# Kernel tuning notes

Hardware: AMD Instinct MI355X
Metric: run time of the kernel (lower is better)

Reference implementation:

```python
import jax, jax.numpy as jnp
import numpy as np

# Config derived from init_kwargs
DIM = 256
DSTATE = 64
DCONV = 3
HEADDIM = 64
CHUNK = 256
NGROUPS = 1
DINNER = int(2.0 * DIM)                 # 512
NHEADS = DINNER // HEADDIM              # 8
CONVDIM = DINNER + 2 * NGROUPS * DSTATE  # 640 (x, B, C share the depthwise conv)
DPROJ = 2 * DINNER + 2 * NGROUPS * DSTATE + NHEADS  # z + xBC + dt


def setup_inputs() -> dict:
    key = jax.random.key(0)
    ks = jax.random.split(key, 8)
    B, H, W = 8, 64, 64
    return dict(
        x=jax.random.normal(ks[0], (B, DIM, H, W), jnp.float32),
        ln_w=jnp.ones((DIM,), jnp.float32),
        ln_b=jnp.zeros((DIM,), jnp.float32),
        in_proj_w=jax.random.normal(ks[1], (DPROJ, DIM), jnp.float32) * 0.02,
        conv_w=jax.random.normal(ks[2], (CONVDIM, 1, DCONV, DCONV), jnp.float32) * 0.1,
        conv_b=jnp.zeros((CONVDIM,), jnp.float32),
        A_log=jnp.log(jax.random.uniform(ks[3], (NHEADS,), jnp.float32, 1.0, 16.0)),
        D=jnp.ones((NHEADS,), jnp.float32),
        dt_bias=jax.random.uniform(ks[4], (NHEADS,), jnp.float32, -2.0, 0.0),
        rms_w=jnp.ones((DINNER,), jnp.float32),
        out_proj_w=jax.random.normal(ks[5], (DIM, DINNER), jnp.float32) * 0.02,
    )


def _ssd(X, dA, Bm, Cm, chunk):
    """Mamba2 SSD chunked parallel scan.
    X:  (b, l, h, p)  inputs already multiplied by dt
    dA: (b, l, h)     dt * A (negative)
    Bm, Cm: (b, l, h, n)
    """
    b, l, h, p = X.shape
    n = Bm.shape[-1]
    c = l // chunk
    q = chunk
    Xc = X.reshape(b, c, q, h, p)
    Bc = Bm.reshape(b, c, q, h, n)
    Cc = Cm.reshape(b, c, q, h, n)
    Ac = dA.reshape(b, c, q, h).transpose(0, 3, 1, 2)            # (b,h,c,q)
    Acs = jnp.cumsum(Ac, axis=-1)                                # (b,h,c,q)
    # intra-chunk (diagonal blocks): causal decay matrix L
    tri = jnp.tril(jnp.ones((q, q), bool))
    Ldec = jnp.where(tri, jnp.exp(Acs[..., :, None] - Acs[..., None, :]), 0.0)
    Y_diag = jnp.einsum('bcqhn,bcshn,bhcqs,bcshp->bcqhp', Cc, Bc, Ldec, Xc)
    # per-chunk final states
    decay_states = jnp.exp(Acs[..., -1:] - Acs)                  # (b,h,c,q)
    states = jnp.einsum('bcqhn,bhcq,bcqhp->bchpn', Bc, decay_states, Xc)
    # inter-chunk recurrence (segment-sum over chunk totals)
    A_last = jnp.pad(Acs[..., -1], ((0, 0), (0, 0), (1, 0)))     # (b,h,c+1)
    ccs = jnp.cumsum(A_last, axis=-1)
    tric = jnp.tril(jnp.ones((c + 1, c + 1), bool))
    decay_chunk = jnp.where(tric, jnp.exp(ccs[..., :, None] - ccs[..., None, :]), 0.0)
    states0 = jnp.concatenate([jnp.zeros_like(states[:, :1]), states], axis=1)
    prev = jnp.einsum('bhzc,bchpn->bzhpn', decay_chunk, states0)[:, :-1]
    # contribution of carried-in state (off-diagonal blocks)
    Y_off = jnp.einsum('bcqhn,bchpn,bhcq->bcqhp', Cc, prev, jnp.exp(Acs))
    return (Y_diag + Y_off).reshape(b, l, h, p)


def _forward(x, ln_w, ln_b, in_proj_w, conv_w, conv_b, A_log, D, dt_bias, rms_w, out_proj_w):
    Bn, Cd, Hh, Ww = x.shape
    L = Hh * Ww
    # LayerNorm over channel dim (channel-first LayerNorm2d)
    mu = jnp.mean(x, axis=1, keepdims=True)
    var = jnp.mean((x - mu) ** 2, axis=1, keepdims=True)
    xn = (x - mu) * jax.lax.rsqrt(var + 1e-5)
    xn = xn * ln_w[None, :, None, None] + ln_b[None, :, None, None]
    # input projection (1x1): -> z | xBC | dt
    zxbcdt = jnp.einsum('bchw,dc->bdhw', xn, in_proj_w)
    z = zxbcdt[:, :DINNER]
    xBC = zxbcdt[:, DINNER:DINNER + CONVDIM]
    dt = zxbcdt[:, DINNER + CONVDIM:]                            # (b, nheads, H, W)
    # depthwise 2D conv + SiLU on xBC
    xBC = jax.lax.conv_general_dilated(
        xBC, conv_w, (1, 1), 'SAME',
        dimension_numbers=('NCHW', 'OIHW', 'NCHW'), feature_group_count=CONVDIM)
    xBC = jax.nn.silu(xBC + conv_b[None, :, None, None])
    # flatten spatial -> sequence, channel-last
    def to_seq(t):
        return t.reshape(Bn, t.shape[1], L).transpose(0, 2, 1)
    xBC, dt, z = to_seq(xBC), to_seq(dt), to_seq(z)
    xs = xBC[..., :DINNER].reshape(Bn, L, NHEADS, HEADDIM)
    Bg = xBC[..., DINNER:DINNER + NGROUPS * DSTATE].reshape(Bn, L, NGROUPS, DSTATE)
    Cg = xBC[..., DINNER + NGROUPS * DSTATE:].reshape(Bn, L, NGROUPS, DSTATE)
    hpg = NHEADS // NGROUPS
    Bm = jnp.repeat(Bg, hpg, axis=2)
    Cm = jnp.repeat(Cg, hpg, axis=2)
    dt = jax.nn.softplus(dt + dt_bias[None, None, :])            # (b, L, nheads)
    A = -jnp.exp(A_log)
    y = _ssd(xs * dt[..., None], dt * A[None, None, :], Bm, Cm, CHUNK)
    y = y + D[None, None, :, None] * xs                          # skip connection
    y = y.reshape(Bn, L, DINNER)
    # gated RMSNorm: norm(y * silu(z)) * w
    y = y * jax.nn.silu(z)
    y = y * jax.lax.rsqrt(jnp.mean(y * y, axis=-1, keepdims=True) + 1e-5) * rms_w
    out = jnp.einsum('bld,cd->blc', y, out_proj_w)
    out = out.transpose(0, 2, 1).reshape(Bn, Cd, Hh, Ww)
    return x + out                                               # residual


def reference(x, ln_w, ln_b, in_proj_w, conv_w, conv_b, A_log, D, dt_bias, rms_w, out_proj_w):
    return _forward(x, ln_w, ln_b, in_proj_w, conv_w, conv_b, A_log, D, dt_bias, rms_w, out_proj_w)
```

## Files before the change

kernel.cpp:

```cpp
#include <hip/hip_runtime.h>
#include <hip/hip_bf16.h>
#include <math.h>

#define DIMC   256
#define LSP    4096
#define BATCH  8
#define DINNER 512
#define NHEADS 8
#define HEADDIM 64
#define DSTATE 64
#define CONVDIM 640
#define DPROJ  1160
#define MPAD   1280
#define CHUNK  256
#define NCHUNK 16

typedef unsigned short u16;
typedef __attribute__((ext_vector_type(8))) unsigned short u16x8;
typedef __attribute__((ext_vector_type(8))) short s16x8;
typedef __attribute__((ext_vector_type(4))) float f32x4;

#define MFMA16(a,b,c) __builtin_amdgcn_mfma_f32_16x16x32_bf16((s16x8)(a),(s16x8)(b),(c),0,0,0)

__device__ __forceinline__ float bf2f(u16 u){ return __uint_as_float(((unsigned int)u)<<16); }
__device__ __forceinline__ u16 f2bf(float f){
  unsigned int x = __float_as_uint(f);
  unsigned int r = (x + 0x7fffu + ((x>>16)&1u)) >> 16;
  return (u16)r;
}
__device__ __forceinline__ float softplusf(float x){ return (x > 20.f) ? x : log1pf(expf(x)); }
__device__ __forceinline__ float siluf(float x){ return x / (1.f + expf(-x)); }
__device__ __forceinline__ u16x8 fscale(u16x8 v, float s){
  u16x8 r;
  #pragma unroll
  for(int j=0;j<8;j++) r[j] = f2bf(bf2f(v[j])*s);
  return r;
}

__global__ void convert_w(const float* __restrict__ src, u16* __restrict__ dst,
                          int total, int valid){
  int i = blockIdx.x*256 + threadIdx.x;
  if (i >= total) return;
  dst[i] = (i < valid) ? f2bf(src[i]) : (u16)0;
}

__global__ void ln_kernel(const float* __restrict__ X, const float* __restrict__ lnw,
                          const float* __restrict__ lnb, u16* __restrict__ XNT) {
  int pos = blockIdx.x*256 + threadIdx.x;
  int b = pos >> 12, l = pos & (LSP-1);
  const float* xb = X + ((size_t)b*DIMC)*LSP + l;
  float sum=0.f, sq=0.f;
  for (int c=0;c<DIMC;c++){ float v=xb[(size_t)c*LSP]; sum+=v; sq+=v*v; }
  float mu = sum*(1.f/DIMC);
  float var = sq*(1.f/DIMC) - mu*mu;
  float rs = rsqrtf(var + 1e-5f);
  u16* ob = XNT + ((size_t)(b*LSP + l))*DIMC;
  for (int c0=0;c0<DIMC;c0+=8){
    u16x8 v8;
    #pragma unroll
    for(int j=0;j<8;j++){
      float v = xb[(size_t)(c0+j)*LSP];
      v8[j] = f2bf((v-mu)*rs*lnw[c0+j] + lnb[c0+j]);
    }
    *(u16x8*)&ob[c0] = v8;
  }
}

__global__ void gemm_zt_mfma(const u16* __restrict__ W, const u16* __restrict__ Bm,
                             u16* __restrict__ ZT){
  __shared__ u16 As[128][32];
  __shared__ u16 Bs[128][32];
  int tid=threadIdx.x, w=tid>>6, lane=tid&63, l15=lane&15, quad=lane>>4;
  int b=blockIdx.z, m0=blockIdx.y*128, n0=blockIdx.x*128;
  const u16* Ab = Bm + ((size_t)b*LSP + m0)*DIMC;
  f32x4 acc[4][4];
  #pragma unroll
  for(int i=0;i<4;i++)
    #pragma unroll
    for(int j=0;j<4;j++) acc[i][j] = (f32x4){0.f,0.f,0.f,0.f};
  for (int k0=0;k0<DIMC;k0+=32){
    __syncthreads();
    {
      int ch = tid*2;
      int r = ch>>2, o=(ch&3)*8;
      *(u16x8*)&As[r][o] = *(const u16x8*)&Ab[(size_t)r*DIMC + k0 + o];
      *(u16x8*)&Bs[r][o] = *(const u16x8*)&W[(size_t)(n0+r)*DIMC + k0 + o];
      ch++; r = ch>>2; o=(ch&3)*8;
      *(u16x8*)&As[r][o] = *(const u16x8*)&Ab[(size_t)r*DIMC + k0 + o];
      *(u16x8*)&Bs[r][o] = *(const u16x8*)&W[(size_t)(n0+r)*DIMC + k0 + o];
    }
    __syncthreads();
    int mrow = (w>>1)*64, ncol=(w&1)*64;
    u16x8 af[4], bfr[4];
    #pragma unroll
    for(int mt=0;mt<4;mt++) af[mt] = *(const u16x8*)&As[mrow+mt*16+l15][quad*8];
    #pragma unroll
    for(int nt=0;nt<4;nt++) bfr[nt] = *(const u16x8*)&Bs[ncol+nt*16+l15][quad*8];
    #pragma unroll
    for(int mt=0;mt<4;mt++)
      #pragma unroll
      for(int nt=0;nt<4;nt++)
        acc[mt][nt]=MFMA16(af[mt],bfr[nt],acc[mt][nt]);
  }
  #pragma unroll
  for(int mt=0;mt<4;mt++)
    #pragma unroll
    for(int nt=0;nt<4;nt++)
      #pragma unroll
      for(int r=0;r<4;r++){
        int l = m0 + (w>>1)*64 + mt*16 + quad*4 + r;
        int d = n0 + (w&1)*64 + nt*16 + l15;
        ZT[((size_t)b*LSP + l)*DINNER + d] = f2bf(acc[mt][nt][r]);
      }
}

__global__ void gemm_xbcdt_mfma(const u16* __restrict__ A, const u16* __restrict__ Bm,
                                u16* __restrict__ XBC, u16* __restrict__ DT){
  __shared__ u16 As[128][32];
  __shared__ u16 Bs[128][32];
  int tid=threadIdx.x, w=tid>>6, lane=tid&63, l15=lane&15, quad=lane>>4;
  int b=blockIdx.z, m0=DINNER + blockIdx.y*128, n0=blockIdx.x*128;
  const u16* Bb = Bm + ((size_t)b*LSP + n0)*DIMC;
  f32x4 acc[4][4];
  #pragma unroll
  for(int i=0;i<4;i++)
    #pragma unroll
    for(int j=0;j<4;j++) acc[i][j] = (f32x4){0.f,0.f,0.f,0.f};
  for (int k0=0;k0<DIMC;k0+=32){
    __syncthreads();
    {
      int ch = tid*2;
      int r = ch>>2, o=(ch&3)*8;
      *(u16x8*)&As[r][o] = *(const u16x8*)&A[(size_t)(m0+r)*DIMC + k0 + o];
      *(u16x8*)&Bs[r][o] = *(const u16x8*)&Bb[(size_t)r*DIMC + k0 + o];
      ch++; r = ch>>2; o=(ch&3)*8;
      *(u16x8*)&As[r][o] = *(const u16x8*)&A[(size_t)(m0+r)*DIMC + k0 + o];
      *(u16x8*)&Bs[r][o] = *(const u16x8*)&Bb[(size_t)r*DIMC + k0 + o];
    }
    __syncthreads();
    int mrow = (w>>1)*64, ncol=(w&1)*64;
    u16x8 af[4], bfr[4];
    #pragma unroll
    for(int mt=0;mt<4;mt++) af[mt] = *(const u16x8*)&As[mrow+mt*16+l15][quad*8];
    #pragma unroll
    for(int nt=0;nt<4;nt++) bfr[nt] = *(const u16x8*)&Bs[ncol+nt*16+l15][quad*8];
    #pragma unroll
    for(int mt=0;mt<4;mt++)
      #pragma unroll
      for(int nt=0;nt<4;nt++)
        acc[mt][nt]=MFMA16(af[mt],bfr[nt],acc[mt][nt]);
  }
  #pragma unroll
  for(int mt=0;mt<4;mt++)
    #pragma unroll
    for(int nt=0;nt<4;nt++)
      #pragma unroll
      for(int r=0;r<4;r++){
        int row = m0 + (w>>1)*64 + mt*16 + quad*4 + r;
        if (row>=DPROJ) continue;
        int col = n0 + (w&1)*64 + nt*16 + l15;
        u16 v = f2bf(acc[mt][nt][r]);
        if (row<DINNER+CONVDIM)   XBC[((size_t)b*CONVDIM+(row-DINNER))*LSP+col]=v;
        else                      DT[((size_t)b*NHEADS+(row-DINNER-CONVDIM))*LSP+col]=v;
      }
}

__global__ void gemm_out_mfma(const u16* __restrict__ A, const u16* __restrict__ Bm,
                              const float* __restrict__ Res, float* __restrict__ Out){
  __shared__ u16 As[128][32];
  __shared__ u16 Bs[128][32];
  int tid=threadIdx.x, w=tid>>6, lane=tid&63, l15=lane&15, quad=lane>>4;
  int b=blockIdx.z, m0=blockIdx.y*128, n0=blockIdx.x*128;
  const u16* Bb = Bm + ((size_t)b*LSP + n0)*DINNER;
  f32x4 acc[4][4];
  #pragma unroll
  for(int i=0;i<4;i++)
    #pragma unroll
    for(int j=0;j<4;j++) acc[i][j] = (f32x4){0.f,0.f,0.f,0.f};
  for (int k0=0;k0<DINNER;k0+=32){
    __syncthreads();
    {
      int ch = tid*2;
      int r = ch>>2, o=(ch&3)*8;
      *(u16x8*)&As[r][o] = *(const u16x8*)&A[(size_t)(m0+r)*DINNER + k0 + o];
      *(u16x8*)&Bs[r][o] = *(const u16x8*)&Bb[(size_t)r*DINNER + k0 + o];
      ch++; r = ch>>2; o=(ch&3)*8;
      *(u16x8*)&As[r][o] = *(const u16x8*)&A[(size_t)(m0+r)*DINNER + k0 + o];
      *(u16x8*)&Bs[r][o] = *(const u16x8*)&Bb[(size_t)r*DINNER + k0 + o];
    }
    __syncthreads();
    int mrow = (w>>1)*64, ncol=(w&1)*64;
    u16x8 af[4], bfr[4];
    #pragma unroll
    for(int mt=0;mt<4;mt++) af[mt] = *(const u16x8*)&As[mrow+mt*16+l15][quad*8];
    #pragma unroll
    for(int nt=0;nt<4;nt++) bfr[nt] = *(const u16x8*)&Bs[ncol+nt*16+l15][quad*8];
    #pragma unroll
    for(int mt=0;mt<4;mt++)
      #pragma unroll
      for(int nt=0;nt<4;nt++)
        acc[mt][nt]=MFMA16(af[mt],bfr[nt],acc[mt][nt]);
  }
  #pragma unroll
  for(int mt=0;mt<4;mt++)
    #pragma unroll
    for(int nt=0;nt<4;nt++)
      #pragma unroll
      for(int r=0;r<4;r++){
        int row = m0 + (w>>1)*64 + mt*16 + quad*4 + r;
        int col = n0 + (w&1)*64 + nt*16 + l15;
        size_t oi = ((size_t)b*DIMC+row)*LSP+col;
        Out[oi] = acc[mt][nt][r] + Res[oi];
      }
}

__global__ void conv_kernel(u16* __restrict__ XBC, const float* __restrict__ CW,
                            const float* __restrict__ CB){
  int ch = blockIdx.x, b = blockIdx.y, tid = threadIdx.x;
  __shared__ float plane[66*66];
  u16* base = XBC + ((size_t)b*CONVDIM + ch)*LSP;
  for (int idx=tid; idx<66*66; idx+=256){
    int yy = idx/66 - 1, xx = idx%66 - 1;
    float v = 0.f;
    if (yy>=0 && yy<64 && xx>=0 && xx<64) v = bf2f(base[yy*64+xx]);
    plane[idx] = v;
  }
  float wg[9];
  #pragma unroll
  for (int t=0;t<9;t++) wg[t] = CW[ch*9+t];
  float bias = CB[ch];
  __syncthreads();
  for (int r=0;r<16;r++){
    int pix = tid + r*256;
    int y = pix>>6, x = pix&63;
    float s=0.f;
    #pragma unroll
    for(int dy=0;dy<3;dy++)
      #pragma unroll
      for(int dx=0;dx<3;dx++) s += plane[(y+dy)*66 + x+dx]*wg[dy*3+dx];
    base[pix] = f2bf(siluf(s + bias));
  }
}

__global__ void ssd_pre_kernel(const u16* __restrict__ DT, const float* __restrict__ A_log,
                               const float* __restrict__ dt_bias, float* __restrict__ ACS,
                               float* __restrict__ DTV, float* __restrict__ DASUM){
  int c=blockIdx.x, h=blockIdx.y, b=blockIdx.z, tid=threadIdx.x;
  __shared__ float acs[CHUNK];
  size_t base = ((size_t)b*NHEADS+h)*LSP + c*CHUNK + tid;
  float raw = bf2f(DT[base]);
  float dtv = softplusf(raw + dt_bias[h]);
  float Ah = -expf(A_log[h]);
  acs[tid] = dtv*Ah;
  __syncthreads();
  for(int o=1;o<256;o<<=1){
    float add=(tid>=o)?acs[tid-o]:0.f;
    __syncthreads(); acs[tid]+=add; __syncthreads();
  }
  ACS[base] = acs[tid];
  DTV[base] = dtv;
  if (tid==CHUNK-1) DASUM[((size_t)b*NHEADS+h)*NCHUNK+c] = acs[tid];
}

__global__ __launch_bounds__(256,4) void ssd_states_mfma(
    const float* __restrict__ ACS, const float* __restrict__ DTV,
    const float* __restrict__ DASUM, const u16* __restrict__ XBC,
    float* __restrict__ STATES){
  int c=blockIdx.x, h=blockIdx.y, b=blockIdx.z;
  int tid=threadIdx.x, w=tid>>6, lane=tid&63, l15=lane&15, quad=lane>>4;
  __shared__ float wdt[CHUNK];
  __shared__ u16 Xw[64][136];
  __shared__ u16 Bn[64][136];
  {
    size_t base = ((size_t)b*NHEADS+h)*LSP + c*CHUNK + tid;
    float atot = DASUM[((size_t)b*NHEADS+h)*NCHUNK+c];
    wdt[tid] = DTV[base]*expf(atot - ACS[base]);
  }
  __syncthreads();
  f32x4 acc[4];
  #pragma unroll
  for(int i=0;i<4;i++) acc[i] = (f32x4){0.f,0.f,0.f,0.f};
  size_t cb = (size_t)c*CHUNK;
  for(int th=0; th<2; th++){
    __syncthreads();
    {
      int n=tid&63, q4=tid>>6;
      const u16* Xg = XBC + ((size_t)b*CONVDIM + h*HEADDIM + n)*LSP + cb + th*128;
      const u16* Bg = XBC + ((size_t)b*CONVDIM + DINNER + n)*LSP + cb + th*128;
      #pragma unroll
      for(int i=0;i<4;i++){
        int o = q4*32+i*8;
        u16x8 v = *(const u16x8*)&Xg[o];
        u16x8 wv;
        #pragma unroll
        for(int j=0;j<8;j++) wv[j]=f2bf(bf2f(v[j])*wdt[th*128+o+j]);
        *(u16x8*)&Xw[n][o]=wv;
        *(u16x8*)&Bn[n][o] = *(const u16x8*)&Bg[o];
      }
    }
    __syncthreads();
    #pragma unroll
    for(int k8=0;k8<4;k8++){
      u16x8 a = *(const u16x8*)&Xw[w*16+l15][k8*32+quad*8];
      #pragma unroll
      for(int nt=0;nt<4;nt++){
        u16x8 bb = *(const u16x8*)&Bn[nt*16+l15][k8*32+quad*8];
        acc[nt]=MFMA16(a,bb,acc[nt]);
      }
    }
  }
  float* dst = STATES + (((size_t)b*NHEADS+h)*NCHUNK+c)*4096;
  #pragma unroll
  for(int nt=0;nt<4;nt++)
    #pragma unroll
    for(int r=0;r<4;r++)
      dst[(w*16+quad*4+r)*64 + nt*16+l15] = acc[nt][r];
}

__global__ void ssd_scan_kernel(const float* __restrict__ STATES, const float* __restrict__ DASUM,
                                u16* __restrict__ PREVB){
  int g = blockIdx.x, h = blockIdx.y, b = blockIdx.z, tid = threadIdx.x;
  int e = g*256 + tid;
  size_t hb = (size_t)b*NHEADS + h;
  size_t base = hb*NCHUNK*4096 + e;
  float s = 0.f;
  for (int cc=0;cc<NCHUNK;cc++){
    PREVB[base + (size_t)cc*4096] = f2bf(s);
    s = s*expf(DASUM[hb*NCHUNK + cc]) + STATES[base + (size_t)cc*4096];
  }
}

__global__ __launch_bounds__(256,4) void ssd_y_mfma(
    const float* __restrict__ ACS, const float* __restrict__ DTV,
    const u16* __restrict__ XBC, const float* __restrict__ Dp,
    const u16* __restrict__ PREVB, u16* __restrict__ YG){
  int bx = blockIdx.x; int c = bx>>2, tb = bx&3;
  int h = blockIdx.y, b = blockIdx.z;
  int tid=threadIdx.x, w=tid>>6, lane=tid&63, l15=lane&15, quad=lane>>4;
  __shared__ float acs[CHUNK];
  __shared__ float dtv[CHUNK];
  __shared__ u16 Ct[64][72];
  __shared__ u16 Bsb[64][72];
  __shared__ u16 Xsb[64][72];
  __shared__ u16 P[4][16][72];
  {
    size_t base = ((size_t)b*NHEADS+h)*LSP + c*CHUNK + tid;
    acs[tid] = ACS[base];
    dtv[tid] = DTV[base];
  }
  {
    int n = tid&63, q4 = tid>>6;
    const u16* Cg = XBC + ((size_t)b*CONVDIM + DINNER + DSTATE + n)*LSP + (size_t)c*CHUNK + tb*64;
    #pragma unroll
    for(int i=0;i<2;i++){
      u16x8 v = *(const u16x8*)&Cg[q4*16+i*8];
      #pragma unroll
      for(int j=0;j<8;j++) Ct[q4*16+i*8+j][n]=v[j];
    }
  }
  __syncthreads();
  f32x4 Y[4];
  #pragma unroll
  for(int i=0;i<4;i++) Y[i]=(f32x4){0.f,0.f,0.f,0.f};
  int trow = w*16 + l15;
  u16x8 ca0 = *(const u16x8*)&Ct[trow][quad*8];
  u16x8 ca1 = *(const u16x8*)&Ct[trow][32+quad*8];
  {
    float ea = expf(acs[tb*64 + trow]);
    u16x8 a0 = fscale(ca0, ea);
    u16x8 a1 = fscale(ca1, ea);
    const u16* Pg = PREVB + (((size_t)b*NHEADS+h)*NCHUNK + c)*4096;
    #pragma unroll
    for(int pt=0;pt<4;pt++){
      u16x8 b0 = *(const u16x8*)&Pg[(pt*16+l15)*64 + quad*8];
      u16x8 b1 = *(const u16x8*)&Pg[(pt*16+l15)*64 + 32 + quad*8];
      Y[pt]=MFMA16(a0,b0,Y[pt]);
      Y[pt]=MFMA16(a1,b1,Y[pt]);
    }
  }
  int tloc = tb*64 + w*16 + quad*4;
  float acst[4];
  #pragma unroll
  for(int r=0;r<4;r++) acst[r] = acs[tloc+r];
  for(int sb=0; sb<=tb; sb++){
    __syncthreads();
    {
      int n=tid&63, q4=tid>>6;
      const u16* Bg = XBC + ((size_t)b*CONVDIM + DINNER + n)*LSP + (size_t)c*CHUNK + sb*64;
      #pragma unroll
      for(int i=0;i<2;i++){
        u16x8 v = *(const u16x8*)&Bg[q4*16+i*8];
        #pragma unroll
        for(int j=0;j<8;j++) Bsb[q4*16+i*8+j][n]=v[j];
      }
      const u16* Xg = XBC + ((size_t)b*CONVDIM + h*HEADDIM + n)*LSP + (size_t)c*CHUNK + sb*64;
      #pragma unroll
      for(int i=0;i<2;i++){
        int o = q4*16+i*8;
        u16x8 v = *(const u16x8*)&Xg[o];
        u16x8 wv;
        #pragma unroll
        for(int j=0;j<8;j++) wv[j] = f2bf(bf2f(v[j])*dtv[sb*64+o+j]);
        *(u16x8*)&Xsb[n][o] = wv;
      }
    }
    __syncthreads();
    f32x4 S[4];
    #pragma unroll
    for(int st=0;st<4;st++) S[st]=(f32x4){0.f,0.f,0.f,0.f};
    #pragma unroll
    for(int st=0;st<4;st++){
      u16x8 b0 = *(const u16x8*)&Bsb[st*16+l15][quad*8];
      u16x8 b1 = *(const u16x8*)&Bsb[st*16+l15][32+quad*8];
      S[st]=MFMA16(ca0,b0,S[st]);
      S[st]=MFMA16(ca1,b1,S[st]);
    }
    if (sb < tb){
      #pragma unroll
      for(int st=0;st<4;st++){
        float as = acs[sb*64 + st*16 + l15];
        #pragma unroll
        for(int r=0;r<4;r++)
          P[w][quad*4+r][st*16+l15] = f2bf(S[st][r]*expf(acst[r]-as));
      }
    } else {
      #pragma unroll
      for(int st=0;st<4;st++){
        int s = sb*64 + st*16 + l15;
        float as = acs[s];
        #pragma unroll
        for(int r=0;r<4;r++){
          float e = (s <= tloc+r) ? expf(acst[r]-as) : 0.f;
          P[w][quad*4+r][st*16+l15] = f2bf(S[st][r]*e);
        }
      }
    }
    u16x8 p0 = *(const u16x8*)&P[w][l15][quad*8];
    u16x8 p1 = *(const u16x8*)&P[w][l15][32+quad*8];
    #pragma unroll
    for(int pt=0;pt<4;pt++){
      u16x8 x0 = *(const u16x8*)&Xsb[pt*16+l15][quad*8];
      u16x8 x1 = *(const u16x8*)&Xsb[pt*16+l15][32+quad*8];
      Y[pt]=MFMA16(p0,x0,Y[pt]);
      Y[pt]=MFMA16(p1,x1,Y[pt]);
    }
  }
  float Dh = Dp[h];
  size_t lbase = (size_t)b*LSP + c*CHUNK + tb*64;
  #pragma unroll
  for(int pt=0;pt<4;pt++){
    #pragma unroll
    for(int r=0;r<4;r++){
      int tl = w*16 + quad*4 + r;
      int p = pt*16 + l15;
      float xdt = bf2f(Xsb[p][tl]);
      float xs = xdt / dtv[tb*64 + tl];
      float y = Y[pt][r] + Dh*xs;
      YG[(lbase + tl)*DINNER + h*HEADDIM + p] = f2bf(y);
    }
  }
}

__global__ void gate_kernel(u16* __restrict__ YG, const u16* __restrict__ ZT,
                            const float* __restrict__ rmsw){
  __shared__ float rw[DINNER];
  int tid = threadIdx.x;
  for (int i=tid;i<DINNER;i+=256) rw[i]=rmsw[i];
  __syncthreads();
  int wv = tid>>6, lane = tid&63;
  size_t row = (size_t)blockIdx.x*4 + wv;
  size_t base = row*DINNER + lane*8;
  u16x8 yv = *(const u16x8*)&YG[base];
  u16x8 zv = *(const u16x8*)&ZT[base];
  float g[8]; float sq=0.f;
  #pragma unroll
  for(int j=0;j<8;j++){
    g[j] = bf2f(yv[j]) * siluf(bf2f(zv[j]));
    sq += g[j]*g[j];
  }
  #pragma unroll
  for(int o=32;o>0;o>>=1) sq += __shfl_xor(sq, o, 64);
  float rinv = rsqrtf(sq*(1.f/DINNER) + 1e-5f);
  u16x8 ov;
  #pragma unroll
  for(int j=0;j<8;j++) ov[j] = f2bf(g[j]*rinv*rw[lane*8+j]);
  *(u16x8*)&YG[base] = ov;
}

extern "C" void kernel_launch(void* const* d_in, const int* in_sizes, int n_in,
                              void* d_out, int out_size, void* d_ws, size_t ws_size,
                              hipStream_t stream) {
  const float* x     = (const float*)d_in[0];
  const float* lnw   = (const float*)d_in[1];
  const float* lnb   = (const float*)d_in[2];
  const float* inpw  = (const float*)d_in[3];
  const float* convw = (const float*)d_in[4];
  const float* convb = (const float*)d_in[5];
  const float* alog  = (const float*)d_in[6];
  const float* Dp    = (const float*)d_in[7];
  const float* dtbi  = (const float*)d_in[8];
  const float* rmsw  = (const float*)d_in[9];
  const float* outw  = (const float*)d_in[10];
  float* out = (float*)d_out;

  char* ws = (char*)d_ws;
  size_t off = 0;
  auto alloc = [&](size_t bytes)->void*{ void* p = ws+off; off += (bytes+255)&~(size_t)255; return p; };
  u16*   WPIN   = (u16*)  alloc((size_t)MPAD*DIMC*2);
  u16*   WPOUT  = (u16*)  alloc((size_t)DIMC*DINNER*2);
  char*  RA     = (char*) alloc((size_t)BATCH*NHEADS*NCHUNK*4096*4);
  u16*   XNT    = (u16*)RA;
  float* STATES = (float*)RA;
  u16*   ZT     = (u16*)  alloc((size_t)BATCH*LSP*DINNER*2);
  u16*   XBC    = (u16*)  alloc((size_t)BATCH*CONVDIM*LSP*2);
  u16*   DTb    = (u16*)  alloc((size_t)BATCH*NHEADS*LSP*2);
  u16*   PREVB  = (u16*)  alloc((size_t)BATCH*NHEADS*NCHUNK*4096*2);
  float* DASUM  = (float*)alloc((size_t)BATCH*NHEADS*NCHUNK*4);
  float* ACS    = (float*)alloc((size_t)BATCH*NHEADS*LSP*4);
  float* DTV    = (float*)alloc((size_t)BATCH*NHEADS*LSP*4);
  u16*   YG     = (u16*)  alloc((size_t)BATCH*LSP*DINNER*2);

  convert_w<<<(MPAD*DIMC+255)/256,256,0,stream>>>(inpw, WPIN, MPAD*DIMC, DPROJ*DIMC);
  convert_w<<<(DIMC*DINNER+255)/256,256,0,stream>>>(outw, WPOUT, DIMC*DINNER, DIMC*DINNER);
  ln_kernel<<<dim3(BATCH*LSP/256),256,0,stream>>>(x,lnw,lnb,XNT);
  gemm_zt_mfma<<<dim3(DINNER/128,LSP/128,BATCH),256,0,stream>>>(WPIN, XNT, ZT);
  gemm_xbcdt_mfma<<<dim3(LSP/128,(MPAD-DINNER)/128,BATCH),256,0,stream>>>(WPIN, XNT, XBC, DTb);
  conv_kernel<<<dim3(CONVDIM,BATCH),256,0,stream>>>(XBC, convw, convb);
  ssd_pre_kernel<<<dim3(NCHUNK,NHEADS,BATCH),256,0,stream>>>(DTb, alog, dtbi, ACS, DTV, DASUM);
  ssd_states_mfma<<<dim3(NCHUNK,NHEADS,BATCH),256,0,stream>>>(ACS,DTV,DASUM,XBC,STATES);
  ssd_scan_kernel<<<dim3(16,NHEADS,BATCH),256,0,stream>>>(STATES,DASUM,PREVB);
  ssd_y_mfma<<<dim3(NCHUNK*4,NHEADS,BATCH),256,0,stream>>>(ACS,DTV,XBC,Dp,PREVB,YG);
  gate_kernel<<<dim3(BATCH*LSP/4),256,0,stream>>>(YG,ZT,rmsw);
  gemm_out_mfma<<<dim3(LSP/128,DIMC/128,BATCH),256,0,stream>>>(WPOUT, YG, x, out);
}
```

Measured before the change: 385.2 us.

## Fuse input projection GEMMs, fold gating into SSD output and RMSNorm into out GEMM

Merges the two input-projection GEMMs into one kernel that stages a 128-row slab of the normalized input in shared memory once and loops over five weight tiles. The separate gate kernel is removed: SiLU gating moves into the SSD output epilogue, the RMSNorm row scale is computed in the output GEMM prologue, and rms_w is folded into the converted output weight. The dt scaling and the exp(cumsum) factor are moved into the P matrix and the epilogue, which avoids rescaling X and C in bf16. The aim is to cut kernel launches and the extra passes over YG and ZT, at the cost of a larger shared-memory footprint, fewer blocks for the input GEMM, and a serial five-tile loop per block.

Result: faster. 366.0 us (-5.0%).

```diff
diff --git a/kernel.cpp b/kernel.cpp
--- a/kernel.cpp
+++ b/kernel.cpp
@@ -30,18 +30,19 @@
 }
 __device__ __forceinline__ float softplusf(float x){ return (x > 20.f) ? x : log1pf(expf(x)); }
 __device__ __forceinline__ float siluf(float x){ return x / (1.f + expf(-x)); }
-__device__ __forceinline__ u16x8 fscale(u16x8 v, float s){
-  u16x8 r;
-  #pragma unroll
-  for(int j=0;j<8;j++) r[j] = f2bf(bf2f(v[j])*s);
-  return r;
-}
 
 __global__ void convert_w(const float* __restrict__ src, u16* __restrict__ dst,
                           int total, int valid){
   int i = blockIdx.x*256 + threadIdx.x;
   if (i >= total) return;
   dst[i] = (i < valid) ? f2bf(src[i]) : (u16)0;
+}
+
+__global__ void convert_w_rms(const float* __restrict__ src, const float* __restrict__ rmsw,
+                              u16* __restrict__ dst){
+  int i = blockIdx.x*256 + threadIdx.x;
+  if (i >= DIMC*DINNER) return;
+  dst[i] = f2bf(src[i] * rmsw[i & (DINNER-1)]);
 }
 
 __global__ void ln_kernel(const float* __restrict__ X, const float* __restrict__ lnw,
@@ -66,112 +67,104 @@
   }
 }
 
-__global__ void gemm_zt_mfma(const u16* __restrict__ W, const u16* __restrict__ Bm,
-                             u16* __restrict__ ZT){
-  __shared__ u16 As[128][32];
-  __shared__ u16 Bs[128][32];
+__global__ __launch_bounds__(256,2) void gemm_in_fused(
+    const u16* __restrict__ W, const u16* __restrict__ XNT,
+    u16* __restrict__ ZT, u16* __restrict__ XBC, u16* __restrict__ DT){
+  __shared__ u16 Xs[128][264];
+  __shared__ u16 Ws[128][32];
   int tid=threadIdx.x, w=tid>>6, lane=tid&63, l15=lane&15, quad=lane>>4;
-  int b=blockIdx.z, m0=blockIdx.y*128, n0=blockIdx.x*128;
-  const u16* Ab = Bm + ((size_t)b*LSP + m0)*DIMC;
-  f32x4 acc[4][4];
-  #pragma unroll
-  for(int i=0;i<4;i++)
-    #pragma unroll
-    for(int j=0;j<4;j++) acc[i][j] = (f32x4){0.f,0.f,0.f,0.f};
-  for (int k0=0;k0<DIMC;k0+=32){
-    __syncthreads();
-    {
-      int ch = tid*2;
-      int r = ch>>2, o=(ch&3)*8;
-      *(u16x8*)&As[r][o] = *(const u16x8*)&Ab[(size_t)r*DIMC + k0 + o];
-      *(u16x8*)&Bs[r][o] = *(const u16x8*)&W[(size_t)(n0+r)*DIMC + k0 + o];
-      ch++; r = ch>>2; o=(ch&3)*8;
-      *(u16x8*)&As[r][o] = *(const u16x8*)&Ab[(size_t)r*DIMC + k0 + o];
-      *(u16x8*)&Bs[r][o] = *(const u16x8*)&W[(size_t)(n0+r)*DIMC + k0 + o];
-    }
-    __syncthreads();
-    int mrow = (w>>1)*64, ncol=(w&1)*64;
-    u16x8 af[4], bfr[4];
-    #pragma unroll
-    for(int mt=0;mt<4;mt++) af[mt] = *(const u16x8*)&As[mrow+mt*16+l15][quad*8];
-    #pragma unroll
-    for(int nt=0;nt<4;nt++) bfr[nt] = *(const u16x8*)&Bs[ncol+nt*16+l15][quad*8];
-    #pragma unroll
-    for(int mt=0;mt<4;mt++)
-      #pragma unroll
-      for(int nt=0;nt<4;nt++)
-        acc[mt][nt]=MFMA16(af[mt],bfr[nt],acc[mt][nt]);
-  }
-  #pragma unroll
-  for(int mt=0;mt<4;mt++)
-    #pragma unroll
-    for(int nt=0;nt<4;nt++)
-      #pragma unroll
-      for(int r=0;r<4;r++){
-        int l = m0 + (w>>1)*64 + mt*16 + quad*4 + r;
-        int d = n0 + (w&1)*64 + nt*16 + l15;
-        ZT[((size_t)b*LSP + l)*DINNER + d] = f2bf(acc[mt][nt][r]);
-      }
-}
-
-__global__ void gemm_xbcdt_mfma(const u16* __restrict__ A, const u16* __restrict__ Bm,
-                                u16* __restrict__ XBC, u16* __restrict__ DT){
-  __shared__ u16 As[128][32];
-  __shared__ u16 Bs[128][32];
-  int tid=threadIdx.x, w=tid>>6, lane=tid&63, l15=lane&15, quad=lane>>4;
-  int b=blockIdx.z, m0=DINNER + blockIdx.y*128, n0=blockIdx.x*128;
-  const u16* Bb = Bm + ((size_t)b*LSP + n0)*DIMC;
-  f32x4 acc[4][4];
-  #pragma unroll
-  for(int i=0;i<4;i++)
-    #pragma unroll
-    for(int j=0;j<4;j++) acc[i][j] = (f32x4){0.f,0.f,0.f,0.f};
-  for (int k0=0;k0<DIMC;k0+=32){
-    __syncthreads();
-    {
-      int ch = tid*2;
-      int r = ch>>2, o=(ch&3)*8;
-      *(u16x8*)&As[r][o] = *(const u16x8*)&A[(size_t)(m0+r)*DIMC + k0 + o];
-      *(u16x8*)&Bs[r][o] = *(const u16x8*)&Bb[(size_t)r*DIMC + k0 + o];
-      ch++; r = ch>>2; o=(ch&3)*8;
-      *(u16x8*)&As[r][o] = *(const u16x8*)&A[(size_t)(m0+r)*DIMC + k0 + o];
-      *(u16x8*)&Bs[r][o] = *(const u16x8*)&Bb[(size_t)r*DIMC + k0 + o];
-    }
-    __syncthreads();
-    int mrow = (w>>1)*64, ncol=(w&1)*64;
-    u16x8 af[4], bfr[4];
-    #pragma unroll
-    for(int mt=0;mt<4;mt++) af[mt] = *(const u16x8*)&As[mrow+mt*16+l15][quad*8];
-    #pragma unroll
-    for(int nt=0;nt<4;nt++) bfr[nt] = *(const u16x8*)&Bs[ncol+nt*16+l15][quad*8];
-    #pragma unroll
-    for(int mt=0;mt<4;mt++)
-      #pragma unroll
-      for(int nt=0;nt<4;nt++)
-        acc[mt][nt]=MFMA16(af[mt],bfr[nt],acc[mt][nt]);
-  }
-  #pragma unroll
-  for(int mt=0;mt<4;mt++)
-    #pragma unroll
-    for(int nt=0;nt<4;nt++)
-      #pragma unroll
-      for(int r=0;r<4;r++){
-        int row = m0 + (w>>1)*64 + mt*16 + quad*4 + r;
-        if (row>=DPROJ) continue;
-        int col = n0 + (w&1)*64 + nt*16 + l15;
-        u16 v = f2bf(acc[mt][nt][r]);
-        if (row<DINNER+CONVDIM)   XBC[((size_t)b*CONVDIM+(row-DINNER))*LSP+col]=v;
-        else                      DT[((size_t)b*NHEADS+(row-DINNER-CONVDIM))*LSP+col]=v;
-      }
+  int n0=blockIdx.x*128, mh=blockIdx.y, b=blockIdx.z;
+  {
+    const u16* src = XNT + ((size_t)(b*LSP + n0))*DIMC;
+    #pragma unroll
+    for (int i=0;i<16;i++){
+      int g = i*256 + tid;
+      int row = g>>5, c8 = (g&31)*8;
+      *(u16x8*)&Xs[row][c8] = *(const u16x8*)&src[(size_t)row*DIMC + c8];
+    }
+  }
+  for (int pti=0; pti<5; pti++){
+    int ptg = mh*5 + pti;
+    int m0 = ptg*128;
+    f32x4 acc[4][4];
+    #pragma unroll
+    for(int i=0;i<4;i++)
+      #pragma unroll
+      for(int j=0;j<4;j++) acc[i][j]=(f32x4){0.f,0.f,0.f,0.f};
+    for (int k0=0;k0<DIMC;k0+=32){
+      __syncthreads();
+      {
+        int ch = tid*2;
+        int r = ch>>2, o=(ch&3)*8;
+        *(u16x8*)&Ws[r][o] = *(const u16x8*)&W[(size_t)(m0+r)*DIMC + k0 + o];
+        ch++; r = ch>>2; o=(ch&3)*8;
+        *(u16x8*)&Ws[r][o] = *(const u16x8*)&W[(size_t)(m0+r)*DIMC + k0 + o];
+      }
+      __syncthreads();
+      u16x8 af[4], bfr[4];
+      if (ptg < 4){
+        #pragma unroll
+        for(int mt=0;mt<4;mt++) af[mt] = *(const u16x8*)&Xs[(w>>1)*64+mt*16+l15][k0+quad*8];
+        #pragma unroll
+        for(int nt=0;nt<4;nt++) bfr[nt] = *(const u16x8*)&Ws[(w&1)*64+nt*16+l15][quad*8];
+      } else {
+        #pragma unroll
+        for(int mt=0;mt<4;mt++) af[mt] = *(const u16x8*)&Ws[(w>>1)*64+mt*16+l15][quad*8];
+        #pragma unroll
+        for(int nt=0;nt<4;nt++) bfr[nt] = *(const u16x8*)&Xs[(w&1)*64+nt*16+l15][k0+quad*8];
+      }
+      #pragma unroll
+      for(int mt=0;mt<4;mt++)
+        #pragma unroll
+        for(int nt=0;nt<4;nt++)
+          acc[mt][nt]=MFMA16(af[mt],bfr[nt],acc[mt][nt]);
+    }
+    if (ptg < 4){
+      #pragma unroll
+      for(int mt=0;mt<4;mt++)
+        #pragma unroll
+        for(int nt=0;nt<4;nt++)
+          #pragma unroll
+          for(int r=0;r<4;r++){
+            int lrow = n0 + (w>>1)*64 + mt*16 + quad*4 + r;
+            int dcol = m0 + (w&1)*64 + nt*16 + l15;
+            ZT[((size_t)b*LSP + lrow)*DINNER + dcol] = f2bf(acc[mt][nt][r]);
+          }
+    } else {
+      #pragma unroll
+      for(int mt=0;mt<4;mt++)
+        #pragma unroll
+        for(int nt=0;nt<4;nt++)
+          #pragma unroll
+          for(int r=0;r<4;r++){
+            int prow = m0 + (w>>1)*64 + mt*16 + quad*4 + r;
+            if (prow>=DPROJ) continue;
+            int col = n0 + (w&1)*64 + nt*16 + l15;
+            u16 v = f2bf(acc[mt][nt][r]);
+            if (prow<DINNER+CONVDIM)  XBC[((size_t)b*CONVDIM+(prow-DINNER))*LSP+col]=v;
+            else                      DT[((size_t)b*NHEADS+(prow-DINNER-CONVDIM))*LSP+col]=v;
+          }
+    }
+  }
 }
 
 __global__ void gemm_out_mfma(const u16* __restrict__ A, const u16* __restrict__ Bm,
                               const float* __restrict__ Res, float* __restrict__ Out){
   __shared__ u16 As[128][32];
   __shared__ u16 Bs[128][32];
+  __shared__ float rinv[128];
   int tid=threadIdx.x, w=tid>>6, lane=tid&63, l15=lane&15, quad=lane>>4;
   int b=blockIdx.z, m0=blockIdx.y*128, n0=blockIdx.x*128;
   const u16* Bb = Bm + ((size_t)b*LSP + n0)*DINNER;
+  for (int rr=w; rr<128; rr+=4){
+    u16x8 v = *(const u16x8*)&Bb[(size_t)rr*DINNER + lane*8];
+    float s=0.f;
+    #pragma unroll
+    for(int j=0;j<8;j++){ float f=bf2f(v[j]); s+=f*f; }
+    #pragma unroll
+    for(int o=32;o>0;o>>=1) s += __shfl_xor(s,o,64);
+    if (lane==0) rinv[rr] = rsqrtf(s*(1.f/DINNER) + 1e-5f);
+  }
   f32x4 acc[4][4];
   #pragma unroll
   for(int i=0;i<4;i++)
@@ -189,12 +182,11 @@
       *(u16x8*)&Bs[r][o] = *(const u16x8*)&Bb[(size_t)r*DINNER + k0 + o];
     }
     __syncthreads();
-    int mrow = (w>>1)*64, ncol=(w&1)*64;
     u16x8 af[4], bfr[4];
     #pragma unroll
-    for(int mt=0;mt<4;mt++) af[mt] = *(const u16x8*)&As[mrow+mt*16+l15][quad*8];
-    #pragma unroll
-    for(int nt=0;nt<4;nt++) bfr[nt] = *(const u16x8*)&Bs[ncol+nt*16+l15][quad*8];
+    for(int mt=0;mt<4;mt++) af[mt] = *(const u16x8*)&As[(w>>1)*64+mt*16+l15][quad*8];
+    #pragma unroll
+    for(int nt=0;nt<4;nt++) bfr[nt] = *(const u16x8*)&Bs[(w&1)*64+nt*16+l15][quad*8];
     #pragma unroll
     for(int mt=0;mt<4;mt++)
       #pragma unroll
@@ -204,14 +196,16 @@
   #pragma unroll
   for(int mt=0;mt<4;mt++)
     #pragma unroll
-    for(int nt=0;nt<4;nt++)
+    for(int nt=0;nt<4;nt++){
+      float rv = rinv[(w&1)*64 + nt*16 + l15];
       #pragma unroll
       for(int r=0;r<4;r++){
         int row = m0 + (w>>1)*64 + mt*16 + quad*4 + r;
         int col = n0 + (w&1)*64 + nt*16 + l15;
         size_t oi = ((size_t)b*DIMC+row)*LSP+col;
-        Out[oi] = acc[mt][nt][r] + Res[oi];
-      }
+        Out[oi] = acc[mt][nt][r]*rv + Res[oi];
+      }
+    }
 }
 
 __global__ void conv_kernel(u16* __restrict__ XBC, const float* __restrict__ CW,
@@ -333,7 +327,8 @@
 __global__ __launch_bounds__(256,4) void ssd_y_mfma(
     const float* __restrict__ ACS, const float* __restrict__ DTV,
     const u16* __restrict__ XBC, const float* __restrict__ Dp,
-    const u16* __restrict__ PREVB, u16* __restrict__ YG){
+    const u16* __restrict__ PREVB, const u16* __restrict__ ZT,
+    u16* __restrict__ YG){
   int bx = blockIdx.x; int c = bx>>2, tb = bx&3;
   int h = blockIdx.y, b = blockIdx.z;
   int tid=threadIdx.x, w=tid>>6, lane=tid&63, l15=lane&15, quad=lane>>4;
@@ -359,23 +354,20 @@
     }
   }
   __syncthreads();
-  f32x4 Y[4];
-  #pragma unroll
-  for(int i=0;i<4;i++) Y[i]=(f32x4){0.f,0.f,0.f,0.f};
+  f32x4 Yd[4], Yo[4];
+  #pragma unroll
+  for(int i=0;i<4;i++){ Yd[i]=(f32x4){0.f,0.f,0.f,0.f}; Yo[i]=(f32x4){0.f,0.f,0.f,0.f}; }
   int trow = w*16 + l15;
   u16x8 ca0 = *(const u16x8*)&Ct[trow][quad*8];
   u16x8 ca1 = *(const u16x8*)&Ct[trow][32+quad*8];
   {
-    float ea = expf(acs[tb*64 + trow]);
-    u16x8 a0 = fscale(ca0, ea);
-    u16x8 a1 = fscale(ca1, ea);
     const u16* Pg = PREVB + (((size_t)b*NHEADS+h)*NCHUNK + c)*4096;
     #pragma unroll
     for(int pt=0;pt<4;pt++){
       u16x8 b0 = *(const u16x8*)&Pg[(pt*16+l15)*64 + quad*8];
       u16x8 b1 = *(const u16x8*)&Pg[(pt*16+l15)*64 + 32 + quad*8];
-      Y[pt]=MFMA16(a0,b0,Y[pt]);
-      Y[pt]=MFMA16(a1,b1,Y[pt]);
+      Yo[pt]=MFMA16(ca0,b0,Yo[pt]);
+      Yo[pt]=MFMA16(ca1,b1,Yo[pt]);
     }
   }
   int tloc = tb*64 + w*16 + quad*4;
@@ -397,11 +389,7 @@
       #pragma unroll
       for(int i=0;i<2;i++){
         int o = q4*16+i*8;
-        u16x8 v = *(const u16x8*)&Xg[o];
-        u16x8 wv;
-        #pragma unroll
-        for(int j=0;j<8;j++) wv[j] = f2bf(bf2f(v[j])*dtv[sb*64+o+j]);
-        *(u16x8*)&Xsb[n][o] = wv;
+        *(u16x8*)&Xsb[n][o] = *(const u16x8*)&Xg[o];
       }
     }
     __syncthreads();
@@ -418,20 +406,23 @@
     if (sb < tb){
       #pragma unroll
       for(int st=0;st<4;st++){
-        float as = acs[sb*64 + st*16 + l15];
+        int s = sb*64 + st*16 + l15;
+        float as = acs[s];
+        float dv = dtv[s];
         #pragma unroll
         for(int r=0;r<4;r++)
-          P[w][quad*4+r][st*16+l15] = f2bf(S[st][r]*expf(acst[r]-as));
+          P[w][quad*4+r][st*16+l15] = f2bf(S[st][r]*expf(acst[r]-as)*dv);
       }
     } else {
       #pragma unroll
       for(int st=0;st<4;st++){
         int s = sb*64 + st*16 + l15;
         float as = acs[s];
+        float dv = dtv[s];
         #pragma unroll
         for(int r=0;r<4;r++){
           float e = (s <= tloc+r) ? expf(acst[r]-as) : 0.f;
-          P[w][quad*4+r][st*16+l15] = f2bf(S[st][r]*e);
+          P[w][quad*4+r][st*16+l15] = f2bf(S[st][r]*e*dv);
         }
       }
     }
@@ -441,11 +432,14 @@
     for(int pt=0;pt<4;pt++){
       u16x8 x0 = *(const u16x8*)&Xsb[pt*16+l15][quad*8];
       u16x8 x1 = *(const u16x8*)&Xsb[pt*16+l15][32+quad*8];
-      Y[pt]=MFMA16(p0,x0,Y[pt]);
-      Y[pt]=MFMA16(p1,x1,Y[pt]);
+      Yd[pt]=MFMA16(p0,x0,Yd[pt]);
+      Yd[pt]=MFMA16(p1,x1,Yd[pt]);
     }
   }
   float Dh = Dp[h];
+  float eat[4];
+  #pragma unroll
+  for(int r=0;r<4;r++) eat[r] = expf(acst[r]);
   size_t lbase = (size_t)b*LSP + c*CHUNK + tb*64;
   #pragma unroll
   for(int pt=0;pt<4;pt++){
@@ -453,38 +447,13 @@
     for(int r=0;r<4;r++){
       int tl = w*16 + quad*4 + r;
       int p = pt*16 + l15;
-      float xdt = bf2f(Xsb[p][tl]);
-      float xs = xdt / dtv[tb*64 + tl];
-      float y = Y[pt][r] + Dh*xs;
-      YG[(lbase + tl)*DINNER + h*HEADDIM + p] = f2bf(y);
-    }
-  }
-}
-
-__global__ void gate_kernel(u16* __restrict__ YG, const u16* __restrict__ ZT,
-                            const float* __restrict__ rmsw){
-  __shared__ float rw[DINNER];
-  int tid = threadIdx.x;
-  for (int i=tid;i<DINNER;i+=256) rw[i]=rmsw[i];
-  __syncthreads();
-  int wv = tid>>6, lane = tid&63;
-  size_t row = (size_t)blockIdx.x*4 + wv;
-  size_t base = row*DINNER + lane*8;
-  u16x8 yv = *(const u16x8*)&YG[base];
-  u16x8 zv = *(const u16x8*)&ZT[base];
-  float g[8]; float sq=0.f;
-  #pragma unroll
-  for(int j=0;j<8;j++){
-    g[j] = bf2f(yv[j]) * siluf(bf2f(zv[j]));
-    sq += g[j]*g[j];
-  }
-  #pragma unroll
-  for(int o=32;o>0;o>>=1) sq += __shfl_xor(sq, o, 64);
-  float rinv = rsqrtf(sq*(1.f/DINNER) + 1e-5f);
-  u16x8 ov;
-  #pragma unroll
-  for(int j=0;j<8;j++) ov[j] = f2bf(g[j]*rinv*rw[lane*8+j]);
-  *(u16x8*)&YG[base] = ov;
+      float xs = bf2f(Xsb[p][tl]);
+      float y = Yd[pt][r] + eat[r]*Yo[pt][r] + Dh*xs;
+      size_t oi = (lbase + tl)*DINNER + h*HEADDIM + p;
+      float zv = bf2f(ZT[oi]);
+      YG[oi] = f2bf(y * siluf(zv));
+    }
+  }
 }
 
 extern "C" void kernel_launch(void* const* d_in, const int* in_sizes, int n_in,
@@ -521,15 +490,13 @@
   u16*   YG     = (u16*)  alloc((size_t)BATCH*LSP*DINNER*2);
 
   convert_w<<<(MPAD*DIMC+255)/256,256,0,stream>>>(inpw, WPIN, MPAD*DIMC, DPROJ*DIMC);
-  convert_w<<<(DIMC*DINNER+255)/256,256,0,stream>>>(outw, WPOUT, DIMC*DINNER, DIMC*DINNER);
+  convert_w_rms<<<(DIMC*DINNER+255)/256,256,0,stream>>>(outw, rmsw, WPOUT);
   ln_kernel<<<dim3(BATCH*LSP/256),256,0,stream>>>(x,lnw,lnb,XNT);
-  gemm_zt_mfma<<<dim3(DINNER/128,LSP/128,BATCH),256,0,stream>>>(WPIN, XNT, ZT);
-  gemm_xbcdt_mfma<<<dim3(LSP/128,(MPAD-DINNER)/128,BATCH),256,0,stream>>>(WPIN, XNT, XBC, DTb);
+  gemm_in_fused<<<dim3(LSP/128,2,BATCH),256,0,stream>>>(WPIN, XNT, ZT, XBC, DTb);
   conv_kernel<<<dim3(CONVDIM,BATCH),256,0,stream>>>(XBC, convw, convb);
   ssd_pre_kernel<<<dim3(NCHUNK,NHEADS,BATCH),256,0,stream>>>(DTb, alog, dtbi, ACS, DTV, DASUM);
   ssd_states_mfma<<<dim3(NCHUNK,NHEADS,BATCH),256,0,stream>>>(ACS,DTV,DASUM,XBC,STATES);
   ssd_scan_kernel<<<dim3(16,NHEADS,BATCH),256,0,stream>>>(STATES,DASUM,PREVB);
-  ssd_y_mfma<<<dim3(NCHUNK*4,NHEADS,BATCH),256,0,stream>>>(ACS,DTV,XBC,Dp,PREVB,YG);
-  gate_kernel<<<dim3(BATCH*LSP/4),256,0,stream>>>(YG,ZT,rmsw);
+  ssd_y_mfma<<<dim3(NCHUNK*4,NHEADS,BATCH),256,0,stream>>>(ACS,DTV,XBC,Dp,PREVB,ZT,YG);
   gemm_out_mfma<<<dim3(LSP/128,DIMC/128,BATCH),256,0,stream>>>(WPOUT, YG, x, out);
 }
```
